# Kernel optimization log

Measured on AMD Instinct MI355X. Metric: run time of the kernel, lower is better.

The kernel has to match this reference:

```python
import jax, jax.numpy as jnp
import numpy as np

D = 1e-16  # matches module-level `d` in the torch source


def setup_inputs() -> dict:
    key = jax.random.key(0)
    k1, k2, k3, k4, k5 = jax.random.split(key, 5)
    B, C, H, W = 8, 64, 192, 320
    x = jax.random.normal(k1, (B, C, H, W), dtype=jnp.float32)
    # physically plausible camera params (scaled uniforms)
    h_cam = 1.2 + 0.6 * jax.random.uniform(k2, (B,), dtype=jnp.float32)
    p_cam = 0.15 + 0.15 * jax.random.uniform(k3, (B,), dtype=jnp.float32)
    fu = 250.0 + 100.0 * jax.random.uniform(k4, (B,), dtype=jnp.float32)
    fv = 250.0 + 100.0 * jax.random.uniform(k5, (B,), dtype=jnp.float32)
    return {"x": x, "h_cam": h_cam, "p_cam": p_cam, "fu": fu, "fv": fv, "plane_height": 0}


def _bev_forward(x, h_cam, p_cam, fu, fv, plane_h):
    B, C, H, W = x.shape
    cu, cv = W / 2.0, H / 2.0
    h_ref = h_cam - plane_h
    sp, cp = jnp.sin(p_cam), jnp.cos(p_cam)
    z = jnp.zeros_like(h_cam)

    # world -> image homography, (B, 3, 3)
    row0 = jnp.stack([cu * cp, -fu, cu * h_ref * sp], -1)
    row1 = jnp.stack([cv * cp - fv * sp, z, h_ref * (fv * cp + cv * sp)], -1)
    row2 = jnp.stack([cp, z, h_ref * sp], -1)
    mats = jnp.stack([row0, row1, row2], 1)

    # BEV scales and centers
    scales = h_cam / (sp * (cv * cp + fv * sp) + D)          # (B,)
    centers = jnp.stack([h_cam * cp / (sp + D), z, jnp.ones_like(h_cam)], -1)  # (B, 3)

    # BEV grid (flattened, row-major over (v, u)), N = H*W
    vv, uu = jnp.meshgrid(jnp.arange(H, dtype=x.dtype), jnp.arange(W, dtype=x.dtype), indexing="ij")
    u = uu.reshape(-1)
    v = vv.reshape(-1)

    # bev_coord -> world_coord
    s = scales[:, None]
    wx = centers[:, 0:1] + s * (cv - v[None, :])   # (B, N)
    wy = centers[:, 1:2] + s * (cu - u[None, :])
    world = jnp.stack([wx, wy, jnp.ones_like(wx)], 1)  # (B, 3, N)

    # world_coord -> image_coord (homogeneous divide)
    uvw = jnp.einsum("bij,bjn->bin", mats, world)
    su = uvw[:, 0] / uvw[:, 2]   # sampled u, (B, N)
    sv = uvw[:, 1] / uvw[:, 2]   # sampled v, (B, N)

    # bilinear interpolation with clamped corner indices (as in the torch code,
    # weights are computed from the CLAMPED integer coordinates)
    u0i = jnp.clip(jnp.floor(su).astype(jnp.int32), 0, W - 1)
    u1i = jnp.clip(jnp.floor(su).astype(jnp.int32) + 1, 0, W - 1)
    v0i = jnp.clip(jnp.floor(sv).astype(jnp.int32), 0, H - 1)
    v1i = jnp.clip(jnp.floor(sv).astype(jnp.int32) + 1, 0, H - 1)
    u0f, u1f = u0i.astype(x.dtype), u1i.astype(x.dtype)
    v0f, v1f = v0i.astype(x.dtype), v1i.astype(x.dtype)

    xf = x.reshape(B, C, H * W)

    def gather(vi, ui):
        idx = vi * W + ui                       # (B, N)
        return jnp.take_along_axis(xf, idx[:, None, :], axis=2)  # (B, C, N)

    wa = ((v1f - sv) * (u1f - su))[:, None, :]
    wb = ((sv - v0f) * (u1f - su))[:, None, :]
    wc = ((v1f - sv) * (su - u0f))[:, None, :]
    wd = ((sv - v0f) * (su - u0f))[:, None, :]

    vals = (wa * gather(v0i, u0i) + wb * gather(v1i, u0i)
            + wc * gather(v0i, u1i) + wd * gather(v1i, u1i))
    out = vals.reshape(B, C, H, W)
    return out, scales, centers


def reference(x, h_cam, p_cam, fu, fv, plane_height):
    return _bev_forward(x, h_cam, p_cam, fu, fv, float(plane_height))
```

## Files before the change

kernel.cpp:

```cpp
#include <hip/hip_runtime.h>

#define B_ 8
#define C_ 64
#define H_ 192
#define W_ 320
#define HW_ (H_*W_)
#define OUT_ELEMS ((size_t)B_*C_*H_*W_)

#define CSPLIT 8
#define CPB    (C_/CSPLIT)
#define PIXT   4

typedef float f32x4 __attribute__((ext_vector_type(4)));

__global__ void bev_setup_kernel(const float* __restrict__ h_cam,
                                 const float* __restrict__ p_cam,
                                 const float* __restrict__ fu,
                                 const float* __restrict__ fv,
                                 const int*   __restrict__ plane_h,
                                 double* __restrict__ params,
                                 float*  __restrict__ scales_out,
                                 float*  __restrict__ centers_out) {
    int b = threadIdx.x;
    if (b >= B_) return;
    const double D  = 1e-16;
    const double cu = W_ / 2.0;
    const double cv = H_ / 2.0;
    double h   = (double)h_cam[b];
    double p   = (double)p_cam[b];
    double dfu = (double)fu[b];
    double dfv = (double)fv[b];
    double ph  = (double)plane_h[0];
    double h_ref = h - ph;
    double sp = sin(p), cp = cos(p);

    double m00 = cu * cp;
    double m01 = -dfu;
    double m02 = cu * h_ref * sp;
    double m10 = cv * cp - dfv * sp;
    double m12 = h_ref * (dfv * cp + cv * sp);
    double m20 = cp;
    double m22 = h_ref * sp;
    double s   = h / (sp * (cv * cp + dfv * sp) + D);
    double cx  = h * cp / (sp + D);

    double* pp = params + (size_t)b * 10;
    pp[0] = m00; pp[1] = m01; pp[2] = m02;
    pp[3] = m10; pp[4] = m12;
    pp[5] = m20; pp[6] = m22;
    pp[7] = s;   pp[8] = cx;

    scales_out[b] = (float)s;
    centers_out[b*3 + 0] = (float)cx;
    centers_out[b*3 + 1] = 0.0f;
    centers_out[b*3 + 2] = 1.0f;
}

__global__ __launch_bounds__(256)
void bev_main_kernel(const float* __restrict__ x,
                     const double* __restrict__ params,
                     float* __restrict__ out) {
    const int bc   = blockIdx.y;
    const int b    = bc >> 3;
    const int c0   = (bc & 7) * CPB;
    const int pix0 = (blockIdx.x * 256 + threadIdx.x) * PIXT;
    const int v    = pix0 / W_;
    const int u    = pix0 - v * W_;

    const double* pp = params + (size_t)b * 10;
    const double m00 = pp[0], m01 = pp[1], m02 = pp[2];
    const double m10 = pp[3], m12 = pp[4];
    const double m20 = pp[5], m22 = pp[6];
    const double s   = pp[7], cx  = pp[8];

    const double wx     = cx + s * ((double)(H_/2) - (double)v);
    const double t2     = m20 * wx + m22;
    const double inv_t2 = 1.0 / t2;
    const double sv     = (m10 * wx + m12) * inv_t2;
    const double su_c   = (m00 * wx + m02) * inv_t2;
    const double su_k   = m01 * s * inv_t2;

    const bool rowin = (sv >= 0.0) && (sv < (double)(H_-1));
    int v0i = 0;
    float dv0 = 0.f, dv1 = 0.f;
    if (rowin) {
        v0i = (int)sv;
        dv0 = (float)(sv - (double)v0i);
        dv1 = (float)((double)(v0i + 1) - sv);
    }

    float wa[PIXT], wb[PIXT], wc[PIXT], wd[PIXT];
    int   base[PIXT];
    #pragma unroll
    for (int k = 0; k < PIXT; ++k) {
        const double su = su_c + su_k * ((double)(W_/2) - (double)(u + k));
        const bool inr = rowin && (su >= 0.0) && (su < (double)(W_-1));
        int u0i = 0;
        float du0 = 0.f, du1 = 0.f;
        if (inr) {
            u0i = (int)su;
            du0 = (float)(su - (double)u0i);
            du1 = (float)((double)(u0i + 1) - su);
        }
        wa[k] = dv1 * du1;
        wb[k] = dv0 * du1;
        wc[k] = dv1 * du0;
        wd[k] = dv0 * du0;
        base[k] = v0i * W_ + u0i;
    }

    const float* __restrict__ xb = x   + ((size_t)(b * C_ + c0)) * HW_;
    float* __restrict__       ob = out + ((size_t)(b * C_ + c0)) * HW_ + (size_t)pix0;

    #pragma unroll 2
    for (int c = 0; c < CPB; ++c) {
        const float* __restrict__ xc = xb + (size_t)c * HW_;
        f32x4 r;
        r.x = wa[0]*xc[base[0]] + wb[0]*xc[base[0]+W_] + wc[0]*xc[base[0]+1] + wd[0]*xc[base[0]+W_+1];
        r.y = wa[1]*xc[base[1]] + wb[1]*xc[base[1]+W_] + wc[1]*xc[base[1]+1] + wd[1]*xc[base[1]+W_+1];
        r.z = wa[2]*xc[base[2]] + wb[2]*xc[base[2]+W_] + wc[2]*xc[base[2]+1] + wd[2]*xc[base[2]+W_+1];
        r.w = wa[3]*xc[base[3]] + wb[3]*xc[base[3]+W_] + wc[3]*xc[base[3]+1] + wd[3]*xc[base[3]+W_+1];
        __builtin_nontemporal_store(r, (f32x4*)(ob + (size_t)c * HW_));
    }
}

extern "C" void kernel_launch(void* const* d_in, const int* in_sizes, int n_in,
                              void* d_out, int out_size, void* d_ws, size_t ws_size,
                              hipStream_t stream) {
    const float* x     = (const float*)d_in[0];
    const float* h_cam = (const float*)d_in[1];
    const float* p_cam = (const float*)d_in[2];
    const float* fu    = (const float*)d_in[3];
    const float* fv    = (const float*)d_in[4];
    const int*   ph    = (const int*)  d_in[5];

    float* out = (float*)d_out;
    float* scales_out  = out + OUT_ELEMS;
    float* centers_out = out + OUT_ELEMS + B_;
    double* params = (double*)d_ws;

    bev_setup_kernel<<<1, 64, 0, stream>>>(h_cam, p_cam, fu, fv, ph,
                                           params, scales_out, centers_out);

    dim3 grid(HW_ / (256 * PIXT), B_ * CSPLIT);
    bev_main_kernel<<<grid, 256, 0, stream>>>(x, params, out);
}
```

Baseline: 46.82 us.

## Stage the two source rows per output row in shared memory

Each BEV output row maps to a single source row pair (v0, v0+1), so the kernel now assigns one block per output row and channel group. The block loads both source rows for 16 channels into LDS with vectorized loads, then does the bilinear gathers from shared memory. This replaces scattered global gathers with coalesced loads and some redundant reads. The cost is a block barrier and about 40KB of LDS per block, which can limit occupancy.

```diff
diff --git a/kernel.cpp b/kernel.cpp
--- a/kernel.cpp
+++ b/kernel.cpp
@@ -7,9 +7,9 @@
 #define HW_ (H_*W_)
 #define OUT_ELEMS ((size_t)B_*C_*H_*W_)
 
-#define CSPLIT 8
+#define CSPLIT 4
 #define CPB    (C_/CSPLIT)
-#define PIXT   4
+#define NTHR   320
 
 typedef float f32x4 __attribute__((ext_vector_type(4)));
 
@@ -56,16 +56,14 @@
     centers_out[b*3 + 2] = 1.0f;
 }
 
-__global__ __launch_bounds__(256)
-void bev_main_kernel(const float* __restrict__ x,
-                     const double* __restrict__ params,
-                     float* __restrict__ out) {
-    const int bc   = blockIdx.y;
-    const int b    = bc >> 3;
-    const int c0   = (bc & 7) * CPB;
-    const int pix0 = (blockIdx.x * 256 + threadIdx.x) * PIXT;
-    const int v    = pix0 / W_;
-    const int u    = pix0 - v * W_;
+__global__ __launch_bounds__(NTHR)
+void bev_row_kernel(const float* __restrict__ x,
+                    const double* __restrict__ params,
+                    float* __restrict__ out) {
+    const int v  = blockIdx.x;
+    const int b  = blockIdx.y >> 2;
+    const int c0 = (blockIdx.y & 3) * CPB;
+    const int t  = threadIdx.x;
 
     const double* pp = params + (size_t)b * 10;
     const double m00 = pp[0], m01 = pp[1], m02 = pp[2];
@@ -89,38 +87,60 @@
         dv1 = (float)((double)(v0i + 1) - sv);
     }
 
-    float wa[PIXT], wb[PIXT], wc[PIXT], wd[PIXT];
-    int   base[PIXT];
+    __shared__ __align__(16) float rows[2][CPB][W_];
+    if (rowin) {
+        const float* __restrict__ src =
+            x + (((size_t)(b * C_ + c0)) * H_ + (size_t)v0i) * W_;
+        #pragma unroll
+        for (int j = 0; j < (2 * CPB * (W_/4)) / NTHR; ++j) {
+            const int i   = t + j * NTHR;
+            const int c   = i / 160;
+            const int rem = i - c * 160;
+            const int rr  = rem / 80;
+            const int q   = rem - rr * 80;
+            const f32x4 val = *(const f32x4*)(src + ((size_t)c * H_ + (size_t)rr) * W_ + (size_t)q * 4);
+            *(f32x4*)&rows[rr][c][q * 4] = val;
+        }
+    }
+    __syncthreads();
+
+    const int p4  = t % 80;
+    const int chg = t / 80;
+    const int u0  = p4 * 4;
+
+    float wA[4], wB[4], wC[4], wD[4];
+    int col[4];
     #pragma unroll
-    for (int k = 0; k < PIXT; ++k) {
-        const double su = su_c + su_k * ((double)(W_/2) - (double)(u + k));
+    for (int k = 0; k < 4; ++k) {
+        const double su = su_c + su_k * ((double)(W_/2) - (double)(u0 + k));
         const bool inr = rowin && (su >= 0.0) && (su < (double)(W_-1));
-        int u0i = 0;
+        int ui = 0;
         float du0 = 0.f, du1 = 0.f;
         if (inr) {
-            u0i = (int)su;
-            du0 = (float)(su - (double)u0i);
-            du1 = (float)((double)(u0i + 1) - su);
+            ui  = (int)su;
+            du0 = (float)(su - (double)ui);
+            du1 = (float)((double)(ui + 1) - su);
         }
-        wa[k] = dv1 * du1;
-        wb[k] = dv0 * du1;
-        wc[k] = dv1 * du0;
-        wd[k] = dv0 * du0;
-        base[k] = v0i * W_ + u0i;
+        wA[k] = dv1 * du1;
+        wB[k] = dv0 * du1;
+        wC[k] = dv1 * du0;
+        wD[k] = dv0 * du0;
+        col[k] = ui;
     }
 
-    const float* __restrict__ xb = x   + ((size_t)(b * C_ + c0)) * HW_;
-    float* __restrict__       ob = out + ((size_t)(b * C_ + c0)) * HW_ + (size_t)pix0;
+    float* __restrict__ ob =
+        out + (((size_t)(b * C_ + c0 + chg * 4)) * H_ + (size_t)v) * W_ + (size_t)u0;
 
-    #pragma unroll 2
-    for (int c = 0; c < CPB; ++c) {
-        const float* __restrict__ xc = xb + (size_t)c * HW_;
+    #pragma unroll
+    for (int cc = 0; cc < 4; ++cc) {
+        const float* __restrict__ r0 = rows[0][chg * 4 + cc];
+        const float* __restrict__ r1 = rows[1][chg * 4 + cc];
         f32x4 r;
-        r.x = wa[0]*xc[base[0]] + wb[0]*xc[base[0]+W_] + wc[0]*xc[base[0]+1] + wd[0]*xc[base[0]+W_+1];
-        r.y = wa[1]*xc[base[1]] + wb[1]*xc[base[1]+W_] + wc[1]*xc[base[1]+1] + wd[1]*xc[base[1]+W_+1];
-        r.z = wa[2]*xc[base[2]] + wb[2]*xc[base[2]+W_] + wc[2]*xc[base[2]+1] + wd[2]*xc[base[2]+W_+1];
-        r.w = wa[3]*xc[base[3]] + wb[3]*xc[base[3]+W_] + wc[3]*xc[base[3]+1] + wd[3]*xc[base[3]+W_+1];
-        __builtin_nontemporal_store(r, (f32x4*)(ob + (size_t)c * HW_));
+        r.x = wA[0]*r0[col[0]] + wC[0]*r0[col[0]+1] + wB[0]*r1[col[0]] + wD[0]*r1[col[0]+1];
+        r.y = wA[1]*r0[col[1]] + wC[1]*r0[col[1]+1] + wB[1]*r1[col[1]] + wD[1]*r1[col[1]+1];
+        r.z = wA[2]*r0[col[2]] + wC[2]*r0[col[2]+1] + wB[2]*r1[col[2]] + wD[2]*r1[col[2]+1];
+        r.w = wA[3]*r0[col[3]] + wC[3]*r0[col[3]+1] + wB[3]*r1[col[3]] + wD[3]*r1[col[3]+1];
+        __builtin_nontemporal_store(r, (f32x4*)(ob + (size_t)cc * HW_));
     }
 }
 
@@ -142,6 +162,6 @@
     bev_setup_kernel<<<1, 64, 0, stream>>>(h_cam, p_cam, fu, fv, ph,
                                            params, scales_out, centers_out);
 
-    dim3 grid(HW_ / (256 * PIXT), B_ * CSPLIT);
-    bev_main_kernel<<<grid, 256, 0, stream>>>(x, params, out);
+    dim3 grid(H_, B_ * CSPLIT);
+    bev_row_kernel<<<grid, NTHR, 0, stream>>>(x, params, out);
 }
```

New measurement: 60.13 us. +28.4%, slower.
